# Performance work log

Hardware: AMD Instinct MI355X
Metric: run time of the kernel (lower is better)

Reference implementation:

```python
import jax, jax.numpy as jnp
import numpy as np

N_USERS = 50000
N_ENTITIES = 100000
N_RELATIONS = 16
N_EDGES = 3200000
NNZ = 2500000
CH = 64
N_HOPS = 2


def l2_normalize(x, eps=1e-12):
    # matches torch F.normalize(dim=1): x / max(||x||_2, eps)
    n = jnp.sqrt(jnp.sum(x * x, axis=-1, keepdims=True))
    return x / jnp.maximum(n, eps)


def setup_inputs() -> dict:
    key = jax.random.key(0)
    ks = jax.random.split(key, 10)
    user_emb = jax.random.normal(ks[0], (N_USERS, CH), dtype=jnp.float32)
    entity_emb = jax.random.normal(ks[1], (N_ENTITIES, CH), dtype=jnp.float32)
    weight = jax.random.normal(ks[2], (N_RELATIONS, CH), dtype=jnp.float32)
    triplet_mask = jax.random.uniform(ks[3], (N_EDGES,), dtype=jnp.float32)
    interact_vals = jnp.ones((NNZ,), dtype=jnp.float32)
    edge_head = jax.random.randint(ks[4], (N_EDGES,), 0, N_ENTITIES, dtype=jnp.int32)
    edge_tail = jax.random.randint(ks[5], (N_EDGES,), 0, N_ENTITIES, dtype=jnp.int32)
    edge_type = jax.random.randint(ks[6], (N_EDGES,), 1, N_RELATIONS + 1, dtype=jnp.int32)
    interact_rows = jax.random.randint(ks[7], (NNZ,), 0, N_USERS, dtype=jnp.int32)
    interact_cols = jax.random.randint(ks[8], (NNZ,), 0, N_ENTITIES, dtype=jnp.int32)
    return {
        'user_emb': user_emb, 'entity_emb': entity_emb, 'weight': weight,
        'triplet_mask': triplet_mask, 'interact_vals': interact_vals,
        'edge_head': edge_head, 'edge_tail': edge_tail, 'edge_type': edge_type,
        'interact_rows': interact_rows, 'interact_cols': interact_cols,
    }


def reference(user_emb, entity_emb, weight, triplet_mask, interact_vals,
              edge_head, edge_tail, edge_type, interact_rows, interact_cols):
    unmask = triplet_mask
    entity_res = entity_emb
    user_res = user_emb
    for _ in range(N_HOPS):
        # KG aggregate: gather tail embeddings, mask + relation multiply, scatter-sum to heads
        neigh = entity_emb[edge_tail] * unmask[:, None] * weight[edge_type - 1]  # [E, CH]
        entity_agg = jax.ops.segment_sum(neigh, edge_head, num_segments=N_ENTITIES)
        # user aggregate: sparse interact_mat @ entity_emb (COO gather + segment_sum)
        user_agg = jax.ops.segment_sum(
            interact_vals[:, None] * entity_emb[interact_cols],
            interact_rows, num_segments=N_USERS)
        # mess_dropout disabled (eval mode -> identity)
        entity_emb = l2_normalize(entity_agg)
        user_emb = l2_normalize(user_agg)
        entity_res = entity_res + entity_emb
        user_res = user_res + user_emb
    return entity_res, user_res
```

## Files before the change

### kernel.cpp

```cpp
#include <hip/hip_runtime.h>

#define N_USERS 50000
#define N_ENTITIES 100000
#define N_RELATIONS 16
#define N_EDGES 3200000
#define NNZ 2500000
#define CH 64

#define RPB 64
#define NB_E 1563
#define NB_U 782
#define NBUCKETS (NB_E + NB_U)
#define STAGE 3840

#define NCE 49
#define NCU 25
#define CAPC_E 67072
#define CAPC_U 104448
#define NCU_DOUT 14

#define PA_KG 256
#define PA_U  192
#define PACK_BLOCKS 1563
#define SE 10
#define SU 16

typedef float v2f __attribute__((ext_vector_type(2)));

__device__ __forceinline__ unsigned short f2bf(float f) {
    unsigned u = __float_as_uint(f);
    u += 0x7FFF + ((u >> 16) & 1);
    return (unsigned short)(u >> 16);
}

__device__ __forceinline__ v2f bfpair(unsigned q) {
    v2f r;
    r.x = __uint_as_float(q << 16);
    r.y = __uint_as_float(q & 0xFFFF0000u);
    return r;
}

__device__ __forceinline__ int wave_incl_scan(int v, int lane) {
    int s = v;
    #pragma unroll
    for (int d = 1; d < 64; d <<= 1) {
        int x = __shfl_up(s, d, 64);
        if (lane >= d) s += x;
    }
    return s;
}

__global__ void __launch_bounds__(1024)
passA_kernel(const int* __restrict__ head, const int* __restrict__ tail,
             const int* __restrict__ type, const float* __restrict__ maskp,
             const int* __restrict__ irows, const int* __restrict__ icols,
             const float* __restrict__ ivals,
             const float4* __restrict__ entity_emb, ushort4* __restrict__ cur_bf,
             int* __restrict__ fineCnt, int* __restrict__ cCurE,
             int* __restrict__ cCurU,
             int2* __restrict__ cbE, int2* __restrict__ cbU_d,
             int2* __restrict__ cbU_w) {
    __shared__ int histF[NB_E];
    __shared__ int histC[64];
    __shared__ int lbase[64];
    __shared__ int2* utab[NCU];
    const int blk = blockIdx.x;
    const int t = threadIdx.x;

    if (blk >= PA_KG + PA_U) {
        const int ne4 = N_ENTITIES * CH / 4;
        int i = (blk - PA_KG - PA_U) * 1024 + t;
        if (i < ne4) {
            float4 v = entity_emb[i];
            ushort4 bq;
            bq.x = f2bf(v.x); bq.y = f2bf(v.y); bq.z = f2bf(v.z); bq.w = f2bf(v.w);
            cur_bf[i] = bq;
        }
        return;
    }

    if (blk < PA_KG) {
        for (int i = t; i < NB_E; i += 1024) histF[i] = 0;
        if (t < NCE) histC[t] = 0;
        __syncthreads();
        const int chunk = (N_EDGES + PA_KG - 1) / PA_KG;
        int base = blk * chunk, lim = min(base + chunk, N_EDGES);
        for (int i = base + t; i < lim; i += 1024) {
            int h = head[i];
            atomicAdd(&histF[h >> 6], 1);
            atomicAdd(&histC[h >> 11], 1);
        }
        __syncthreads();
        for (int i = t; i < NB_E; i += 1024)
            if (histF[i]) atomicAdd(&fineCnt[NB_U + i], histF[i]);
        if (t < NCE) {
            int c = histC[t];
            lbase[t] = c ? atomicAdd(&cCurE[t], c) : 0;
            histC[t] = 0;
        }
        __syncthreads();
        int i = base + t;
        for (; i + 3072 < lim; i += 4096) {
            int i0 = i, i1 = i + 1024, i2 = i + 2048, i3 = i + 3072;
            int h0 = head[i0], h1 = head[i1], h2 = head[i2], h3 = head[i3];
            int x0 = tail[i0] | ((type[i0] - 1) << 17) | ((h0 & 63) << 21) | (((h0 >> 6) & 31) << 27);
            int x1 = tail[i1] | ((type[i1] - 1) << 17) | ((h1 & 63) << 21) | (((h1 >> 6) & 31) << 27);
            int x2 = tail[i2] | ((type[i2] - 1) << 17) | ((h2 & 63) << 21) | (((h2 >> 6) & 31) << 27);
            int x3 = tail[i3] | ((type[i3] - 1) << 17) | ((h3 & 63) << 21) | (((h3 >> 6) & 31) << 27);
            float m0 = maskp[i0], m1 = maskp[i1], m2 = maskp[i2], m3 = maskp[i3];
            int c0 = h0 >> 11, c1 = h1 >> 11, c2 = h2 >> 11, c3 = h3 >> 11;
            int l0 = lbase[c0] + atomicAdd(&histC[c0], 1);
            int l1 = lbase[c1] + atomicAdd(&histC[c1], 1);
            int l2 = lbase[c2] + atomicAdd(&histC[c2], 1);
            int l3 = lbase[c3] + atomicAdd(&histC[c3], 1);
            if (l0 < CAPC_E) cbE[(size_t)c0 * CAPC_E + l0] = make_int2(x0, __float_as_int(m0));
            if (l1 < CAPC_E) cbE[(size_t)c1 * CAPC_E + l1] = make_int2(x1, __float_as_int(m1));
            if (l2 < CAPC_E) cbE[(size_t)c2 * CAPC_E + l2] = make_int2(x2, __float_as_int(m2));
            if (l3 < CAPC_E) cbE[(size_t)c3 * CAPC_E + l3] = make_int2(x3, __float_as_int(m3));
        }
        for (; i < lim; i += 1024) {
            int h = head[i];
            int x = tail[i] | ((type[i] - 1) << 17) | ((h & 63) << 21) | (((h >> 6) & 31) << 27);
            int c = h >> 11;
            int loc = lbase[c] + atomicAdd(&histC[c], 1);
            if (loc < CAPC_E)
                cbE[(size_t)c * CAPC_E + loc] = make_int2(x, __float_as_int(maskp[i]));
        }
    } else {
        if (t < NCU)
            utab[t] = (t < NCU_DOUT) ? (cbU_d + (size_t)t * CAPC_U)
                                     : (cbU_w + (size_t)(t - NCU_DOUT) * CAPC_U);
        for (int i = t; i < NB_U; i += 1024) histF[i] = 0;
        if (t < NCU) histC[t] = 0;
        __syncthreads();
        const int ub = blk - PA_KG;
        const int chunk = (NNZ + PA_U - 1) / PA_U;
        int base = ub * chunk, lim = min(base + chunk, NNZ);
        for (int i = base + t; i < lim; i += 1024) {
            int r = irows[i];
            atomicAdd(&histF[r >> 6], 1);
            atomicAdd(&histC[r >> 11], 1);
        }
        __syncthreads();
        for (int i = t; i < NB_U; i += 1024)
            if (histF[i]) atomicAdd(&fineCnt[i], histF[i]);
        if (t < NCU) {
            int c = histC[t];
            lbase[t] = c ? atomicAdd(&cCurU[t], c) : 0;
            histC[t] = 0;
        }
        __syncthreads();
        int i = base + t;
        for (; i + 3072 < lim; i += 4096) {
            int i0 = i, i1 = i + 1024, i2 = i + 2048, i3 = i + 3072;
            int r0 = irows[i0], r1 = irows[i1], r2 = irows[i2], r3 = irows[i3];
            int x0 = icols[i0] | ((r0 & 63) << 17) | (((r0 >> 6) & 31) << 27);
            int x1 = icols[i1] | ((r1 & 63) << 17) | (((r1 >> 6) & 31) << 27);
            int x2 = icols[i2] | ((r2 & 63) << 17) | (((r2 >> 6) & 31) << 27);
            int x3 = icols[i3] | ((r3 & 63) << 17) | (((r3 >> 6) & 31) << 27);
            float v0 = ivals[i0], v1 = ivals[i1], v2 = ivals[i2], v3 = ivals[i3];
            int c0 = r0 >> 11, c1 = r1 >> 11, c2 = r2 >> 11, c3 = r3 >> 11;
            int l0 = lbase[c0] + atomicAdd(&histC[c0], 1);
            int l1 = lbase[c1] + atomicAdd(&histC[c1], 1);
            int l2 = lbase[c2] + atomicAdd(&histC[c2], 1);
            int l3 = lbase[c3] + atomicAdd(&histC[c3], 1);
            if (l0 < CAPC_U) utab[c0][l0] = make_int2(x0, __float_as_int(v0));
            if (l1 < CAPC_U) utab[c1][l1] = make_int2(x1, __float_as_int(v1));
            if (l2 < CAPC_U) utab[c2][l2] = make_int2(x2, __float_as_int(v2));
            if (l3 < CAPC_U) utab[c3][l3] = make_int2(x3, __float_as_int(v3));
        }
        for (; i < lim; i += 1024) {
            int r = irows[i];
            int x = icols[i] | ((r & 63) << 17) | (((r >> 6) & 31) << 27);
            int c = r >> 11;
            int loc = lbase[c] + atomicAdd(&histC[c], 1);
            if (loc < CAPC_U) utab[c][loc] = make_int2(x, __float_as_int(ivals[i]));
        }
    }
}

__global__ void __launch_bounds__(512)
scan_kernel(const int* __restrict__ fineCnt, int* __restrict__ fineBase,
            int* __restrict__ fineCur) {
    __shared__ int wsums[8];
    __shared__ int carry_s;
    const int t = threadIdx.x, w = t >> 6, lane = t & 63;
    if (t == 0) carry_s = 0;
    __syncthreads();
    for (int base = 0; base < NBUCKETS; base += 512) {
        int i = base + t;
        int v = (i < NBUCKETS) ? fineCnt[i] : 0;
        int s = wave_incl_scan(v, lane);
        if (lane == 63) wsums[w] = s;
        __syncthreads();
        int carry = carry_s;
        if (w == 0) {
            int ws = (lane < 8) ? wsums[lane] : 0;
            int ss = wave_incl_scan(ws, lane);
            if (lane < 8) wsums[lane] = ss - ws;
        }
        __syncthreads();
        int excl = s - v + wsums[w] + carry;
        if (i < NBUCKETS) { fineBase[i] = excl; fineCur[i] = excl; }
        __syncthreads();
        if (t == 511) carry_s = excl + v;
        __syncthreads();
    }
}

__global__ void __launch_bounds__(1024)
passB_kernel(const int* __restrict__ cCurE, const int* __restrict__ cCurU,
             const int2* __restrict__ cbE, const int2* __restrict__ cbU_d,
             const int2* __restrict__ cbU_w,
             int* __restrict__ fineCur, int2* __restrict__ binAll) {
    __shared__ int h32[32];
    __shared__ int lb[32];
    const int blk = blockIdx.x, t = threadIdx.x;
    const int2* __restrict__ src;
    int cnt, sub, S, fid0;
    if (blk < NCE * SE) {
        int c = blk / SE; sub = blk % SE; S = SE;
        cnt = min(cCurE[c], CAPC_E);
        src = cbE + (size_t)c * CAPC_E;
        fid0 = NB_U + c * 32;
    } else {
        int c = (blk - NCE * SE) / SU; sub = (blk - NCE * SE) % SU; S = SU;
        cnt = min(cCurU[c], CAPC_U);
        src = (c < NCU_DOUT) ? cbU_d + (size_t)c * CAPC_U
                             : cbU_w + (size_t)(c - NCU_DOUT) * CAPC_U;
        fid0 = c * 32;
    }
    int len = (cnt + S - 1) / S;
    int b0 = sub * len, b1 = min(b0 + len, cnt);
    if (t < 32) h32[t] = 0;
    __syncthreads();
    for (int i = b0 + t; i < b1; i += 1024)
        atomicAdd(&h32[(src[i].x >> 27) & 31], 1);
    __syncthreads();
    if (t < 32) {
        int c2 = h32[t];
        lb[t] = c2 ? atomicAdd(&fineCur[fid0 + t], c2) : 0;
        h32[t] = 0;
    }
    __syncthreads();
    int i = b0 + t;
    for (; i + 3072 < b1; i += 4096) {
        int2 e0 = src[i], e1 = src[i + 1024], e2 = src[i + 2048], e3 = src[i + 3072];
        int f0 = (e0.x >> 27) & 31, f1 = (e1.x >> 27) & 31;
        int f2 = (e2.x >> 27) & 31, f3 = (e3.x >> 27) & 31;
        int l0 = lb[f0] + atomicAdd(&h32[f0], 1);
        int l1 = lb[f1] + atomicAdd(&h32[f1], 1);
        int l2 = lb[f2] + atomicAdd(&h32[f2], 1);
        int l3 = lb[f3] + atomicAdd(&h32[f3], 1);
        binAll[l0] = e0; binAll[l1] = e1; binAll[l2] = e2; binAll[l3] = e3;
    }
    for (; i < b1; i += 1024) {
        int2 e = src[i];
        int f = (e.x >> 27) & 31;
        binAll[lb[f] + atomicAdd(&h32[f], 1)] = e;
    }
}

__global__ void __launch_bounds__(512)
sort_kernel(int2* __restrict__ binAll, const int* __restrict__ fineCnt,
            const int* __restrict__ fineBase, int* __restrict__ rowptr) {
    __shared__ int2 sbuf[STAGE];
    __shared__ int  hist[RPB];
    __shared__ int  offs[RPB + 1];

    const int b = blockIdx.x;
    const int t = threadIdx.x;
    const bool is_user = (b < NB_U);
    const int base = fineBase[b];
    int2* __restrict__ bin = binAll + base;
    const int cnt = min(fineCnt[b], STAGE);
    const int rsh = is_user ? 17 : 21;

    if (t < RPB) hist[t] = 0;
    __syncthreads();
    for (int i = t; i < cnt; i += 512)
        atomicAdd(&hist[(bin[i].x >> rsh) & 63], 1);
    __syncthreads();
    if (t < 64) {
        int v = hist[t];
        int s = wave_incl_scan(v, t);
        offs[t] = s - v;
        if (t == 63) offs[64] = s;
    }
    __syncthreads();
    if (t < RPB) hist[t] = 0;
    __syncthreads();
    for (int i = t; i < cnt; i += 512) {
        int2 p = bin[i];
        int r = (p.x >> rsh) & 63;
        int k = atomicAdd(&hist[r], 1);
        sbuf[offs[r] + k] = p;
    }
    __syncthreads();
    for (int i = t; i < cnt; i += 512) bin[i] = sbuf[i];
    if (t <= 64) rowptr[b * 65 + t] = base + offs[t];
}

__global__ void __launch_bounds__(256)
agg_kernel(const uint2* __restrict__ cur64,
           const float* __restrict__ weight,
           const int2* __restrict__ binAll, const int* __restrict__ rowptr,
           unsigned short* __restrict__ nxt,
           const float4* __restrict__ src_e, const float4* __restrict__ src_u,
           float* __restrict__ res_e, float* __restrict__ res_u) {
    __shared__ float4 wl4[N_RELATIONS * 16];
    __shared__ int    srp[33];

    const int hb = blockIdx.x;
    const int b = hb >> 1;
    const int half = hb & 1;
    const int t = threadIdx.x;
    const int w = t >> 6;
    const int lane = t & 63;
    const int g = lane >> 4;
    const int c2 = lane & 15;
    const bool is_user = (b < NB_U);
    const int eb = b - NB_U;

    if (!is_user)
        for (int i = t; i < N_RELATIONS * 16; i += 256)
            wl4[i] = ((const float4*)weight)[i];
    if (t < 33) srp[t] = rowptr[b * 65 + half * 32 + t];
    __syncthreads();

    #pragma unroll
    for (int rr = 0; rr < 8; ++rr) {
        const int row_l = (w << 3) + rr;
        const int s = srp[row_l], e = srp[row_l + 1];
        v2f a01 = {0.f, 0.f}, a23 = {0.f, 0.f};
        int i = s;
        if (is_user) {
            for (; i + 15 < e; i += 16) {
                int2 pa = binAll[i + g];
                int2 pb = binAll[i + 4 + g];
                int2 pc = binAll[i + 8 + g];
                int2 pd = binAll[i + 12 + g];
                uint2 qa = cur64[(size_t)(pa.x & 0x1FFFF) * 16 + c2];
                uint2 qb = cur64[(size_t)(pb.x & 0x1FFFF) * 16 + c2];
                uint2 qc = cur64[(size_t)(pc.x & 0x1FFFF) * 16 + c2];
                uint2 qd = cur64[(size_t)(pd.x & 0x1FFFF) * 16 + c2];
                float sa = __int_as_float(pa.y);
                float sb = __int_as_float(pb.y);
                float sc = __int_as_float(pc.y);
                float sd = __int_as_float(pd.y);
                a01 += bfpair(qa.x) * sa;  a23 += bfpair(qa.y) * sa;
                a01 += bfpair(qb.x) * sb;  a23 += bfpair(qb.y) * sb;
                a01 += bfpair(qc.x) * sc;  a23 += bfpair(qc.y) * sc;
                a01 += bfpair(qd.x) * sd;  a23 += bfpair(qd.y) * sd;
            }
            for (; i + 7 < e; i += 8) {
                int2 pa = binAll[i + g];
                int2 pb = binAll[i + 4 + g];
                uint2 qa = cur64[(size_t)(pa.x & 0x1FFFF) * 16 + c2];
                uint2 qb = cur64[(size_t)(pb.x & 0x1FFFF) * 16 + c2];
                float sa = __int_as_float(pa.y);
                float sb = __int_as_float(pb.y);
                a01 += bfpair(qa.x) * sa;  a23 += bfpair(qa.y) * sa;
                a01 += bfpair(qb.x) * sb;  a23 += bfpair(qb.y) * sb;
            }
            for (; i < e; i += 4) {
                int idx = i + g;
                bool vld = idx < e;
                int2 p = binAll[vld ? idx : i];
                uint2 q = cur64[(size_t)(p.x & 0x1FFFF) * 16 + c2];
                float sv = vld ? __int_as_float(p.y) : 0.f;
                a01 += bfpair(q.x) * sv;  a23 += bfpair(q.y) * sv;
            }
        } else {
            for (; i + 15 < e; i += 16) {
                int2 pa = binAll[i + g];
                int2 pb = binAll[i + 4 + g];
                int2 pc = binAll[i + 8 + g];
                int2 pd = binAll[i + 12 + g];
                uint2 qa = cur64[(size_t)(pa.x & 0x1FFFF) * 16 + c2];
                uint2 qb = cur64[(size_t)(pb.x & 0x1FFFF) * 16 + c2];
                uint2 qc = cur64[(size_t)(pc.x & 0x1FFFF) * 16 + c2];
                uint2 qd = cur64[(size_t)(pd.x & 0x1FFFF) * 16 + c2];
                float4 wa = wl4[((pa.x >> 17) & 15) * 16 + c2];
                float4 wb = wl4[((pb.x >> 17) & 15) * 16 + c2];
                float4 wc = wl4[((pc.x >> 17) & 15) * 16 + c2];
                float4 wd = wl4[((pd.x >> 17) & 15) * 16 + c2];
                float sa = __int_as_float(pa.y);
                float sb = __int_as_float(pb.y);
                float sc = __int_as_float(pc.y);
                float sd = __int_as_float(pd.y);
                v2f wa01 = {wa.x, wa.y}, wa23 = {wa.z, wa.w};
                v2f wb01 = {wb.x, wb.y}, wb23 = {wb.z, wb.w};
                v2f wc01 = {wc.x, wc.y}, wc23 = {wc.z, wc.w};
                v2f wd01 = {wd.x, wd.y}, wd23 = {wd.z, wd.w};
                a01 += bfpair(qa.x) * (wa01 * sa);  a23 += bfpair(qa.y) * (wa23 * sa);
                a01 += bfpair(qb.x) * (wb01 * sb);  a23 += bfpair(qb.y) * (wb23 * sb);
                a01 += bfpair(qc.x) * (wc01 * sc);  a23 += bfpair(qc.y) * (wc23 * sc);
                a01 += bfpair(qd.x) * (wd01 * sd);  a23 += bfpair(qd.y) * (wd23 * sd);
            }
            for (; i + 7 < e; i += 8) {
                int2 pa = binAll[i + g];
                int2 pb = binAll[i + 4 + g];
                uint2 qa = cur64[(size_t)(pa.x & 0x1FFFF) * 16 + c2];
                uint2 qb = cur64[(size_t)(pb.x & 0x1FFFF) * 16 + c2];
                float4 wa = wl4[((pa.x >> 17) & 15) * 16 + c2];
                float4 wb = wl4[((pb.x >> 17) & 15) * 16 + c2];
                float sa = __int_as_float(pa.y);
                float sb = __int_as_float(pb.y);
                v2f wa01 = {wa.x, wa.y}, wa23 = {wa.z, wa.w};
                v2f wb01 = {wb.x, wb.y}, wb23 = {wb.z, wb.w};
                a01 += bfpair(qa.x) * (wa01 * sa);  a23 += bfpair(qa.y) * (wa23 * sa);
                a01 += bfpair(qb.x) * (wb01 * sb);  a23 += bfpair(qb.y) * (wb23 * sb);
            }
            for (; i < e; i += 4) {
                int idx = i + g;
                bool vld = idx < e;
                int2 p = binAll[vld ? idx : i];
                uint2 q = cur64[(size_t)(p.x & 0x1FFFF) * 16 + c2];
                float4 wv = wl4[((p.x >> 17) & 15) * 16 + c2];
                float sv = vld ? __int_as_float(p.y) : 0.f;
                v2f wv01 = {wv.x, wv.y}, wv23 = {wv.z, wv.w};
                a01 += bfpair(q.x) * (wv01 * sv);  a23 += bfpair(q.y) * (wv23 * sv);
            }
        }

        float x0 = a01.x, x1 = a01.y, x2 = a23.x, x3 = a23.y;
        x0 += __shfl_xor(x0, 16, 64); x0 += __shfl_xor(x0, 32, 64);
        x1 += __shfl_xor(x1, 16, 64); x1 += __shfl_xor(x1, 32, 64);
        x2 += __shfl_xor(x2, 16, 64); x2 += __shfl_xor(x2, 32, 64);
        x3 += __shfl_xor(x3, 16, 64); x3 += __shfl_xor(x3, 32, 64);
        float ss = x0 * x0 + x1 * x1 + x2 * x2 + x3 * x3;
        #pragma unroll
        for (int o = 8; o; o >>= 1) ss += __shfl_xor(ss, o, 64);
        float inv = 1.f / fmaxf(sqrtf(ss), 1e-12f);
        float y0 = x0 * inv, y1 = x1 * inv, y2 = x2 * inv, y3 = x3 * inv;
        if (g == 0) {
            const int lrow = half * 32 + row_l;
            if (is_user) {
                int grow = b * RPB + lrow;
                if (grow < N_USERS) {
                    float4 v = src_u[(size_t)grow * 16 + c2];
                    v.x += y0; v.y += y1; v.z += y2; v.w += y3;
                    ((float4*)res_u)[(size_t)grow * 16 + c2] = v;
                }
            } else {
                int grow = eb * RPB + lrow;
                if (grow < N_ENTITIES) {
                    uint2 pk;
                    pk.x = (unsigned)f2bf(y0) | ((unsigned)f2bf(y1) << 16);
                    pk.y = (unsigned)f2bf(y2) | ((unsigned)f2bf(y3) << 16);
                    ((uint2*)nxt)[(size_t)grow * 16 + c2] = pk;
                    float4 v = src_e[(size_t)grow * 16 + c2];
                    v.x += y0; v.y += y1; v.z += y2; v.w += y3;
                    ((float4*)res_e)[(size_t)grow * 16 + c2] = v;
                }
            }
        }
    }
}

extern "C" void kernel_launch(void* const* d_in, const int* in_sizes, int n_in,
                              void* d_out, int out_size, void* d_ws, size_t ws_size,
                              hipStream_t stream) {
    const float* user_emb   = (const float*)d_in[0];
    const float* entity_emb = (const float*)d_in[1];
    const float* weight     = (const float*)d_in[2];
    const float* mask       = (const float*)d_in[3];
    const float* ivals      = (const float*)d_in[4];
    const int*   edge_head  = (const int*)d_in[5];
    const int*   edge_tail  = (const int*)d_in[6];
    const int*   edge_type  = (const int*)d_in[7];
    const int*   irows      = (const int*)d_in[8];
    const int*   icols      = (const int*)d_in[9];

    float* out_entity = (float*)d_out;
    float* out_user   = (float*)d_out + (size_t)N_ENTITIES * CH;

    int2* cbE   = (int2*)d_out;
    int2* cbU_d = cbE + (size_t)NCE * CAPC_E;

    unsigned short* curA = (unsigned short*)d_ws;
    unsigned short* curB = curA + (size_t)N_ENTITIES * CH;
    int2* binAll = (int2*)(curB + (size_t)N_ENTITIES * CH);
    int2* cbU_w  = binAll + (size_t)(N_EDGES + NNZ);
    int*  fineCnt  = (int*)(cbU_w + (size_t)(NCU - NCU_DOUT) * CAPC_U);
    int*  cCurE    = fineCnt + NBUCKETS;
    int*  cCurU    = cCurE + NCE;
    int*  fineBase = cCurU + NCU;
    int*  fineCur  = fineBase + NBUCKETS;
    int*  rowptr   = fineCur + NBUCKETS;

    hipMemsetAsync(fineCnt, 0, (size_t)(NBUCKETS + NCE + NCU) * sizeof(int), stream);

    passA_kernel<<<PA_KG + PA_U + PACK_BLOCKS, 1024, 0, stream>>>(
        edge_head, edge_tail, edge_type, mask, irows, icols, ivals,
        (const float4*)entity_emb, (ushort4*)curA,
        fineCnt, cCurE, cCurU, cbE, cbU_d, cbU_w);

    scan_kernel<<<1, 512, 0, stream>>>(fineCnt, fineBase, fineCur);

    passB_kernel<<<NCE * SE + NCU * SU, 1024, 0, stream>>>(
        cCurE, cCurU, cbE, cbU_d, cbU_w, fineCur, binAll);

    sort_kernel<<<NBUCKETS, 512, 0, stream>>>(binAll, fineCnt, fineBase, rowptr);

    agg_kernel<<<2 * NBUCKETS, 256, 0, stream>>>(
        (const uint2*)curA, weight, binAll, rowptr, curB,
        (const float4*)entity_emb, (const float4*)user_emb,
        out_entity, out_user);
    agg_kernel<<<2 * NBUCKETS, 256, 0, stream>>>(
        (const uint2*)curB, weight, binAll, rowptr, curA,
        (const float4*)out_entity, (const float4*)out_user,
        out_entity, out_user);
}
```

Before: 483.3 us.

## Fuse bucket sort with first-hop aggregation using staged shared-memory edges

Merges the per-bucket sort kernel with the first hop's aggregation kernel. Each block keeps its edges in registers across the histogram and scatter passes instead of re-reading them from global memory, then aggregates rows directly from the sorted shared-memory buffer instead of re-reading the sorted bins. This removes one kernel launch and a global round trip of the edge list. In exchange each block handles 64 rows with 8 waves instead of split half-blocks, and shared-memory use per block grows, which may reduce parallelism and occupancy for the first hop.

```diff
diff --git a/kernel.cpp b/kernel.cpp
--- a/kernel.cpp
+++ b/kernel.cpp
@@ -262,24 +262,42 @@
 }
 
 __global__ void __launch_bounds__(512)
-sort_kernel(int2* __restrict__ binAll, const int* __restrict__ fineCnt,
-            const int* __restrict__ fineBase, int* __restrict__ rowptr) {
-    __shared__ int2 sbuf[STAGE];
-    __shared__ int  hist[RPB];
-    __shared__ int  offs[RPB + 1];
+sortagg_kernel(int2* __restrict__ binAll, const int* __restrict__ fineCnt,
+               const int* __restrict__ fineBase, int* __restrict__ rowptr,
+               const uint2* __restrict__ cur64, const float* __restrict__ weight,
+               unsigned short* __restrict__ nxt,
+               const float4* __restrict__ src_e, const float4* __restrict__ src_u,
+               float* __restrict__ res_e, float* __restrict__ res_u) {
+    __shared__ int2   sbuf[STAGE];
+    __shared__ float4 wl4[N_RELATIONS * 16];
+    __shared__ int    hist[RPB];
+    __shared__ int    offs[RPB + 1];
 
     const int b = blockIdx.x;
     const int t = threadIdx.x;
     const bool is_user = (b < NB_U);
+    const int eb = b - NB_U;
     const int base = fineBase[b];
     int2* __restrict__ bin = binAll + base;
     const int cnt = min(fineCnt[b], STAGE);
     const int rsh = is_user ? 17 : 21;
 
+    int2 ebuf[8];
     if (t < RPB) hist[t] = 0;
-    __syncthreads();
-    for (int i = t; i < cnt; i += 512)
-        atomicAdd(&hist[(bin[i].x >> rsh) & 63], 1);
+    #pragma unroll
+    for (int j = 0; j < 8; ++j) {
+        int idx = t + (j << 9);
+        if (idx < cnt) ebuf[j] = bin[idx];
+    }
+    if (!is_user)
+        for (int i = t; i < N_RELATIONS * 16; i += 512)
+            wl4[i] = ((const float4*)weight)[i];
+    __syncthreads();
+    #pragma unroll
+    for (int j = 0; j < 8; ++j) {
+        int idx = t + (j << 9);
+        if (idx < cnt) atomicAdd(&hist[(ebuf[j].x >> rsh) & 63], 1);
+    }
     __syncthreads();
     if (t < 64) {
         int v = hist[t];
@@ -290,15 +308,152 @@
     __syncthreads();
     if (t < RPB) hist[t] = 0;
     __syncthreads();
-    for (int i = t; i < cnt; i += 512) {
-        int2 p = bin[i];
-        int r = (p.x >> rsh) & 63;
-        int k = atomicAdd(&hist[r], 1);
-        sbuf[offs[r] + k] = p;
+    #pragma unroll
+    for (int j = 0; j < 8; ++j) {
+        int idx = t + (j << 9);
+        if (idx < cnt) {
+            int r = (ebuf[j].x >> rsh) & 63;
+            int k = atomicAdd(&hist[r], 1);
+            sbuf[offs[r] + k] = ebuf[j];
+        }
     }
     __syncthreads();
     for (int i = t; i < cnt; i += 512) bin[i] = sbuf[i];
     if (t <= 64) rowptr[b * 65 + t] = base + offs[t];
+
+    const int w = t >> 6;
+    const int lane = t & 63;
+    const int g = lane >> 4;
+    const int c2 = lane & 15;
+
+    #pragma unroll
+    for (int rr = 0; rr < 8; ++rr) {
+        const int row = (w << 3) + rr;
+        const int s = offs[row], e = offs[row + 1];
+        v2f a01 = {0.f, 0.f}, a23 = {0.f, 0.f};
+        int i = s;
+        if (is_user) {
+            for (; i + 15 < e; i += 16) {
+                int2 pa = sbuf[i + g];
+                int2 pb = sbuf[i + 4 + g];
+                int2 pc = sbuf[i + 8 + g];
+                int2 pd = sbuf[i + 12 + g];
+                uint2 qa = cur64[(size_t)(pa.x & 0x1FFFF) * 16 + c2];
+                uint2 qb = cur64[(size_t)(pb.x & 0x1FFFF) * 16 + c2];
+                uint2 qc = cur64[(size_t)(pc.x & 0x1FFFF) * 16 + c2];
+                uint2 qd = cur64[(size_t)(pd.x & 0x1FFFF) * 16 + c2];
+                float sa = __int_as_float(pa.y);
+                float sb = __int_as_float(pb.y);
+                float sc = __int_as_float(pc.y);
+                float sd = __int_as_float(pd.y);
+                a01 += bfpair(qa.x) * sa;  a23 += bfpair(qa.y) * sa;
+                a01 += bfpair(qb.x) * sb;  a23 += bfpair(qb.y) * sb;
+                a01 += bfpair(qc.x) * sc;  a23 += bfpair(qc.y) * sc;
+                a01 += bfpair(qd.x) * sd;  a23 += bfpair(qd.y) * sd;
+            }
+            for (; i + 7 < e; i += 8) {
+                int2 pa = sbuf[i + g];
+                int2 pb = sbuf[i + 4 + g];
+                uint2 qa = cur64[(size_t)(pa.x & 0x1FFFF) * 16 + c2];
+                uint2 qb = cur64[(size_t)(pb.x & 0x1FFFF) * 16 + c2];
+                float sa = __int_as_float(pa.y);
+                float sb = __int_as_float(pb.y);
+                a01 += bfpair(qa.x) * sa;  a23 += bfpair(qa.y) * sa;
+                a01 += bfpair(qb.x) * sb;  a23 += bfpair(qb.y) * sb;
+            }
+            for (; i < e; i += 4) {
+                int idx = i + g;
+                bool vld = idx < e;
+                int2 p = sbuf[vld ? idx : i];
+                uint2 q = cur64[(size_t)(p.x & 0x1FFFF) * 16 + c2];
+                float sv = vld ? __int_as_float(p.y) : 0.f;
+                a01 += bfpair(q.x) * sv;  a23 += bfpair(q.y) * sv;
+            }
+        } else {
+            for (; i + 15 < e; i += 16) {
+                int2 pa = sbuf[i + g];
+                int2 pb = sbuf[i + 4 + g];
+                int2 pc = sbuf[i + 8 + g];
+                int2 pd = sbuf[i + 12 + g];
+                uint2 qa = cur64[(size_t)(pa.x & 0x1FFFF) * 16 + c2];
+                uint2 qb = cur64[(size_t)(pb.x & 0x1FFFF) * 16 + c2];
+                uint2 qc = cur64[(size_t)(pc.x & 0x1FFFF) * 16 + c2];
+                uint2 qd = cur64[(size_t)(pd.x & 0x1FFFF) * 16 + c2];
+                float4 wa = wl4[((pa.x >> 17) & 15) * 16 + c2];
+                float4 wb = wl4[((pb.x >> 17) & 15) * 16 + c2];
+                float4 wc = wl4[((pc.x >> 17) & 15) * 16 + c2];
+                float4 wd = wl4[((pd.x >> 17) & 15) * 16 + c2];
+                float sa = __int_as_float(pa.y);
+                float sb = __int_as_float(pb.y);
+                float sc = __int_as_float(pc.y);
+                float sd = __int_as_float(pd.y);
+                v2f wa01 = {wa.x, wa.y}, wa23 = {wa.z, wa.w};
+                v2f wb01 = {wb.x, wb.y}, wb23 = {wb.z, wb.w};
+                v2f wc01 = {wc.x, wc.y}, wc23 = {wc.z, wc.w};
+                v2f wd01 = {wd.x, wd.y}, wd23 = {wd.z, wd.w};
+                a01 += bfpair(qa.x) * (wa01 * sa);  a23 += bfpair(qa.y) * (wa23 * sa);
+                a01 += bfpair(qb.x) * (wb01 * sb);  a23 += bfpair(qb.y) * (wb23 * sb);
+                a01 += bfpair(qc.x) * (wc01 * sc);  a23 += bfpair(qc.y) * (wc23 * sc);
+                a01 += bfpair(qd.x) * (wd01 * sd);  a23 += bfpair(qd.y) * (wd23 * sd);
+            }
+            for (; i + 7 < e; i += 8) {
+                int2 pa = sbuf[i + g];
+                int2 pb = sbuf[i + 4 + g];
+                uint2 qa = cur64[(size_t)(pa.x & 0x1FFFF) * 16 + c2];
+                uint2 qb = cur64[(size_t)(pb.x & 0x1FFFF) * 16 + c2];
+                float4 wa = wl4[((pa.x >> 17) & 15) * 16 + c2];
+                float4 wb = wl4[((pb.x >> 17) & 15) * 16 + c2];
+                float sa = __int_as_float(pa.y);
+                float sb = __int_as_float(pb.y);
+                v2f wa01 = {wa.x, wa.y}, wa23 = {wa.z, wa.w};
+                v2f wb01 = {wb.x, wb.y}, wb23 = {wb.z, wb.w};
+                a01 += bfpair(qa.x) * (wa01 * sa);  a23 += bfpair(qa.y) * (wa23 * sa);
+                a01 += bfpair(qb.x) * (wb01 * sb);  a23 += bfpair(qb.y) * (wb23 * sb);
+            }
+            for (; i < e; i += 4) {
+                int idx = i + g;
+                bool vld = idx < e;
+                int2 p = sbuf[vld ? idx : i];
+                uint2 q = cur64[(size_t)(p.x & 0x1FFFF) * 16 + c2];
+                float4 wv = wl4[((p.x >> 17) & 15) * 16 + c2];
+                float sv = vld ? __int_as_float(p.y) : 0.f;
+                v2f wv01 = {wv.x, wv.y}, wv23 = {wv.z, wv.w};
+                a01 += bfpair(q.x) * (wv01 * sv);  a23 += bfpair(q.y) * (wv23 * sv);
+            }
+        }
+
+        float x0 = a01.x, x1 = a01.y, x2 = a23.x, x3 = a23.y;
+        x0 += __shfl_xor(x0, 16, 64); x0 += __shfl_xor(x0, 32, 64);
+        x1 += __shfl_xor(x1, 16, 64); x1 += __shfl_xor(x1, 32, 64);
+        x2 += __shfl_xor(x2, 16, 64); x2 += __shfl_xor(x2, 32, 64);
+        x3 += __shfl_xor(x3, 16, 64); x3 += __shfl_xor(x3, 32, 64);
+        float ss = x0 * x0 + x1 * x1 + x2 * x2 + x3 * x3;
+        #pragma unroll
+        for (int o = 8; o; o >>= 1) ss += __shfl_xor(ss, o, 64);
+        float inv = 1.f / fmaxf(sqrtf(ss), 1e-12f);
+        float y0 = x0 * inv, y1 = x1 * inv, y2 = x2 * inv, y3 = x3 * inv;
+        if (g == 0) {
+            if (is_user) {
+                int grow = b * RPB + row;
+                if (grow < N_USERS) {
+                    float4 v = src_u[(size_t)grow * 16 + c2];
+                    v.x += y0; v.y += y1; v.z += y2; v.w += y3;
+                    ((float4*)res_u)[(size_t)grow * 16 + c2] = v;
+                }
+            } else {
+                int grow = eb * RPB + row;
+                if (grow < N_ENTITIES) {
+                    uint2 pk;
+                    pk.x = (unsigned)f2bf(y0) | ((unsigned)f2bf(y1) << 16);
+                    pk.y = (unsigned)f2bf(y2) | ((unsigned)f2bf(y3) << 16);
+                    ((uint2*)nxt)[(size_t)grow * 16 + c2] = pk;
+                    float4 v = src_e[(size_t)grow * 16 + c2];
+                    v.x += y0; v.y += y1; v.z += y2; v.w += y3;
+                    ((float4*)res_e)[(size_t)grow * 16 + c2] = v;
+                }
+            }
+        }
+    }
 }
 
 __global__ void __launch_bounds__(256)
@@ -502,12 +657,12 @@
     passB_kernel<<<NCE * SE + NCU * SU, 1024, 0, stream>>>(
         cCurE, cCurU, cbE, cbU_d, cbU_w, fineCur, binAll);
 
-    sort_kernel<<<NBUCKETS, 512, 0, stream>>>(binAll, fineCnt, fineBase, rowptr);
-
-    agg_kernel<<<2 * NBUCKETS, 256, 0, stream>>>(
-        (const uint2*)curA, weight, binAll, rowptr, curB,
+    sortagg_kernel<<<NBUCKETS, 512, 0, stream>>>(
+        binAll, fineCnt, fineBase, rowptr,
+        (const uint2*)curA, weight, curB,
         (const float4*)entity_emb, (const float4*)user_emb,
         out_entity, out_user);
+
     agg_kernel<<<2 * NBUCKETS, 256, 0, stream>>>(
         (const uint2*)curB, weight, binAll, rowptr, curA,
         (const float4*)out_entity, (const float4*)out_user,
```

Measured after the change: 452.1 us, median of 2. 6.5% less time.
